# Kernel optimization log

Measured on AMD Instinct MI355X. Metric: run time of the kernel, lower is better.

## Reference

```python
import jax, jax.numpy as jnp
import numpy as np

N = 100000
E = 1600000
F_DIM = 128
H_DIM = 64
K_CLUSTERS = 16
NEG_SLOPE = 0.2


def setup_inputs() -> dict:
    key = jax.random.key(0)
    ks = jax.random.split(key, 10)
    X = jax.random.normal(ks[0], (N, F_DIM), dtype=jnp.float32)
    ei_feat = jax.random.randint(ks[1], (2, E), 0, N, dtype=jnp.int64)
    batch = jnp.zeros((N,), dtype=jnp.int64)
    # GATv2Conv layer 1 params (heads=1): lin_l, lin_r [F,H], att [H], bias [H]
    s1 = 1.0 / np.sqrt(F_DIM)
    W1l = jax.random.uniform(ks[2], (F_DIM, H_DIM), jnp.float32, -s1, s1)
    W1r = jax.random.uniform(ks[3], (F_DIM, H_DIM), jnp.float32, -s1, s1)
    a1 = jax.random.uniform(ks[4], (H_DIM,), jnp.float32, -1/np.sqrt(H_DIM), 1/np.sqrt(H_DIM))
    b1 = jnp.zeros((H_DIM,), jnp.float32)
    # layer 2: [H,K]
    s2 = 1.0 / np.sqrt(H_DIM)
    W2l = jax.random.uniform(ks[5], (H_DIM, K_CLUSTERS), jnp.float32, -s2, s2)
    W2r = jax.random.uniform(ks[6], (H_DIM, K_CLUSTERS), jnp.float32, -s2, s2)
    a2 = jax.random.uniform(ks[7], (K_CLUSTERS,), jnp.float32, -1/np.sqrt(K_CLUSTERS), 1/np.sqrt(K_CLUSTERS))
    b2 = jnp.zeros((K_CLUSTERS,), jnp.float32)
    return {"X": X, "ei_feat": ei_feat, "batch": batch,
            "W1l": W1l, "W1r": W1r, "a1": a1, "b1": b1,
            "W2l": W2l, "W2r": W2r, "a2": a2, "b2": b2}


def gatv2_conv(x, src, dst, Wl, Wr, a, b, n_nodes):
    # GATv2 (heads=1): e_ij = a^T LeakyReLU(Wl x_j + Wr x_i); softmax over j->i; out_i = sum alpha * Wl x_j
    xl = x @ Wl            # [N,H] source transform
    xr = x @ Wr            # [N,H] target transform
    e = jax.nn.leaky_relu(xl[src] + xr[dst], NEG_SLOPE) @ a   # [E']
    m = jax.ops.segment_max(e, dst, num_segments=n_nodes)      # stable softmax per target
    w = jnp.exp(e - m[dst])
    denom = jax.ops.segment_sum(w, dst, num_segments=n_nodes)
    alpha = w / denom[dst]  # every node has a self-loop, so denom > 0
    out = jax.ops.segment_sum(alpha[:, None] * xl[src], dst, num_segments=n_nodes)
    return out + b


def reference(X, ei_feat, batch, W1l, W1r, a1, b1, W2l, W2r, a2, b2):
    loop = jnp.arange(N, dtype=ei_feat.dtype)
    src = jnp.concatenate([ei_feat[0], loop])  # add_self_loops=True (PyG default)
    dst = jnp.concatenate([ei_feat[1], loop])
    h = jax.nn.elu(gatv2_conv(X, src, dst, W1l, W1r, a1, b1, N))
    z = gatv2_conv(h, src, dst, W2l, W2r, a2, b2, N)
    return jax.nn.softmax(z, axis=1)
```

## Files before the change

### kernel.cpp

```cpp
#include <hip/hip_runtime.h>
#include <stdint.h>

#define F_DIM 128
#define H_DIM 64
#define K_DIM 16
#define BUK_SH 8
#define NCH 256

typedef _Float16 half2v __attribute__((ext_vector_type(2)));
typedef _Float16 half4 __attribute__((ext_vector_type(4)));
typedef _Float16 f16x8 __attribute__((ext_vector_type(8)));
typedef float f32x4 __attribute__((ext_vector_type(4)));

__global__ __launch_bounds__(256) void k_hist(const int* __restrict__ dst,
                                              int* __restrict__ hist,
                                              int E, int CH, int NBUK) {
    __shared__ int h[512];
    int t = threadIdx.x, c = blockIdx.x;
    for (int i = t; i < NBUK; i += 256) h[i] = 0;
    __syncthreads();
    int s = c * CH, e = min(s + CH, E);
    for (int i = s + t; i < e; i += 256) atomicAdd(&h[dst[i] >> BUK_SH], 1);
    __syncthreads();
    for (int i = t; i < NBUK; i += 256) hist[i * NCH + c] = h[i];
}

__global__ __launch_bounds__(256) void k_scanBkt(int* __restrict__ hist,
                                                 int* __restrict__ bktTot) {
    __shared__ int sh[256];
    int b = blockIdx.x, t = threadIdx.x;
    int v = hist[b * NCH + t];
    sh[t] = v;
    __syncthreads();
    for (int off = 1; off < 256; off <<= 1) {
        int x = (t >= off) ? sh[t - off] : 0;
        __syncthreads();
        sh[t] += x;
        __syncthreads();
    }
    hist[b * NCH + t] = sh[t] - v;
    if (t == 255) bktTot[b] = sh[255];
}

__global__ __launch_bounds__(256) void k_scanTot(const int* __restrict__ bktTot,
                                                 int* __restrict__ bktBase, int NBUK) {
    __shared__ int sh[256];
    int t = threadIdx.x;
    int i0 = 2 * t, i1 = 2 * t + 1;
    int v0 = (i0 < NBUK) ? bktTot[i0] : 0;
    int v1 = (i1 < NBUK) ? bktTot[i1] : 0;
    int s = v0 + v1;
    sh[t] = s;
    __syncthreads();
    for (int off = 1; off < 256; off <<= 1) {
        int x = (t >= off) ? sh[t - off] : 0;
        __syncthreads();
        sh[t] += x;
        __syncthreads();
    }
    int excl = sh[t] - s;
    if (i0 < NBUK) bktBase[i0] = excl;
    if (i1 < NBUK) bktBase[i1] = excl + v0;
    if (t == 255) bktBase[NBUK] = sh[255];
}

__global__ __launch_bounds__(256) void k_scatter(const int* __restrict__ src,
                                                 const int* __restrict__ dst,
                                                 const int* __restrict__ hist,
                                                 const int* __restrict__ bktBase,
                                                 uint32_t* __restrict__ binned,
                                                 int E, int CH, int NBUK) {
    __shared__ int ctr[512];
    int t = threadIdx.x, c = blockIdx.x;
    for (int i = t; i < NBUK; i += 256) ctr[i] = bktBase[i] + hist[i * NCH + c];
    __syncthreads();
    int s = c * CH, e = min(s + CH, E);
    for (int i = s + t; i < e; i += 256) {
        int d = dst[i];
        int pos = atomicAdd(&ctr[d >> BUK_SH], 1);
        binned[pos] = (uint32_t)src[i] | ((uint32_t)(d & 255) << 20);
    }
}

__global__ __launch_bounds__(256) void k_fine2(const uint32_t* __restrict__ binned,
                                               const int* __restrict__ bktBase,
                                               int* __restrict__ rowptr,
                                               int* __restrict__ col, int N) {
    __shared__ int h[256], sc[256], slotL[256];
    int b = blockIdx.x, t = threadIdx.x;
    int n0 = b << BUK_SH;
    int s = bktBase[b], e = bktBase[b + 1];
    h[t] = 0;
    __syncthreads();
    for (int i = s + t; i < e; i += 256) atomicAdd(&h[binned[i] >> 20], 1);
    __syncthreads();
    int v = h[t];
    sc[t] = v;
    __syncthreads();
    for (int off = 1; off < 256; off <<= 1) {
        int x = (t >= off) ? sc[t - off] : 0;
        __syncthreads();
        sc[t] += x;
        __syncthreads();
    }
    int excl = sc[t] - v;
    int n = n0 + t;
    int rowbase = s + n0;
    if (n < N) {
        int rp = rowbase + excl + t;
        rowptr[n] = rp;
        col[rp] = n;
        slotL[t] = rp + 1;
        if (n == N - 1) rowptr[N] = rp + v + 1;
    }
    __syncthreads();
    for (int i = s + t; i < e; i += 256) {
        uint32_t p = binned[i];
        int pos = atomicAdd(&slotL[p >> 20], 1);
        col[pos] = (int)(p & 0xFFFFFu);
    }
}

__global__ __launch_bounds__(256) void k_gemm1m(
        const float* __restrict__ X,
        const float* __restrict__ W1l, const float* __restrict__ W1r,
        _Float16* __restrict__ xlh, _Float16* __restrict__ xrh, int N) {
    __shared__ _Float16 Ws[16384];
    __shared__ _Float16 Xs[128 * 136];
    int t = threadIdx.x;
    int n0 = blockIdx.x * 128;
    int validRows = N - n0; if (validRows > 128) validRows = 128;
    for (int i = t; i < 4096; i += 256) {
        int k = i >> 5, c4 = (i & 31) << 2;
        float4 v = (c4 < 64) ? *(const float4*)&W1l[k * 64 + c4]
                             : *(const float4*)&W1r[k * 64 + (c4 - 64)];
        int s = k >> 5, q = (k >> 3) & 3, j = k & 7;
        float vv[4] = {v.x, v.y, v.z, v.w};
#pragma unroll
        for (int u = 0; u < 4; ++u) {
            int C = c4 + u, c = C >> 4, n = C & 15;
            Ws[(((c * 4 + s) * 4 + q) * 16 + n) * 8 + j] = (_Float16)vv[u];
        }
    }
    for (int i = t; i < 4096; i += 256) {
        int r = i >> 5, c4 = (i & 31) << 2;
        float4 v = {0.f, 0.f, 0.f, 0.f};
        if (r < validRows) v = *(const float4*)&X[(long)(n0 + r) * 128 + c4];
        half4 hv;
        hv.x = (_Float16)v.x; hv.y = (_Float16)v.y;
        hv.z = (_Float16)v.z; hv.w = (_Float16)v.w;
        *(half4*)&Xs[r * 136 + c4] = hv;
    }
    __syncthreads();
    int w = t >> 6, lane = t & 63;
    int m = lane & 15, q = lane >> 4;
    f32x4 acc[2][8];
#pragma unroll
    for (int a = 0; a < 2; ++a)
#pragma unroll
        for (int c = 0; c < 8; ++c) acc[a][c] = (f32x4){0.f, 0.f, 0.f, 0.f};
#pragma unroll
    for (int s = 0; s < 4; ++s) {
        f16x8 a0 = *(const f16x8*)&Xs[(w * 32 + m) * 136 + s * 32 + q * 8];
        f16x8 a1 = *(const f16x8*)&Xs[(w * 32 + 16 + m) * 136 + s * 32 + q * 8];
#pragma unroll
        for (int c = 0; c < 8; ++c) {
            f16x8 b = *(const f16x8*)&Ws[(((c * 4 + s) * 4 + q) * 16 + m) * 8];
            acc[0][c] = __builtin_amdgcn_mfma_f32_16x16x32_f16(a0, b, acc[0][c], 0, 0, 0);
            acc[1][c] = __builtin_amdgcn_mfma_f32_16x16x32_f16(a1, b, acc[1][c], 0, 0, 0);
        }
    }
#pragma unroll
    for (int sub = 0; sub < 2; ++sub)
#pragma unroll
    for (int c = 0; c < 8; ++c)
#pragma unroll
    for (int r = 0; r < 4; ++r) {
        int gn = n0 + w * 32 + sub * 16 + q * 4 + r;
        if (gn < N) {
            int C = c * 16 + m;
            _Float16 v = (_Float16)acc[sub][c][r];
            if (C < 64) xlh[(long)gn * 64 + C] = v;
            else        xrh[(long)gn * 64 + (C - 64)] = v;
        }
    }
}

__global__ __launch_bounds__(256) void k_gemm2m(
        const _Float16* __restrict__ Hm,
        const float* __restrict__ W2l, const float* __restrict__ W2r,
        _Float16* __restrict__ xlh, _Float16* __restrict__ xrh, int N) {
    __shared__ _Float16 Ws2[2048];
    __shared__ _Float16 Hs[256 * 72];
    int t = threadIdx.x;
    int n0 = blockIdx.x * 256;
    int validRows = N - n0; if (validRows > 256) validRows = 256;
    for (int i = t; i < 512; i += 256) {
        int k = i >> 3, c4 = (i & 7) << 2;
        float4 v = (c4 < 16) ? *(const float4*)&W2l[k * 16 + c4]
                             : *(const float4*)&W2r[k * 16 + (c4 - 16)];
        int s = k >> 5, q = (k >> 3) & 3, j = k & 7;
        float vv[4] = {v.x, v.y, v.z, v.w};
#pragma unroll
        for (int u = 0; u < 4; ++u) {
            int C = c4 + u, c = C >> 4, n = C & 15;
            Ws2[(((c * 2 + s) * 4 + q) * 16 + n) * 8 + j] = (_Float16)vv[u];
        }
    }
    for (int i = t; i < 2048; i += 256) {
        int r = i >> 3, c8 = (i & 7) << 3;
        f16x8 v = {0, 0, 0, 0, 0, 0, 0, 0};
        if (r < validRows) v = *(const f16x8*)&Hm[(long)(n0 + r) * 64 + c8];
        *(f16x8*)&Hs[r * 72 + c8] = v;
    }
    __syncthreads();
    int w = t >> 6, lane = t & 63;
    int m = lane & 15, q = lane >> 4;
    f32x4 acc[4][2];
#pragma unroll
    for (int a = 0; a < 4; ++a)
#pragma unroll
        for (int c = 0; c < 2; ++c) acc[a][c] = (f32x4){0.f, 0.f, 0.f, 0.f};
#pragma unroll
    for (int s = 0; s < 2; ++s) {
        f16x8 a[4];
#pragma unroll
        for (int sub = 0; sub < 4; ++sub)
            a[sub] = *(const f16x8*)&Hs[(w * 64 + sub * 16 + m) * 72 + s * 32 + q * 8];
#pragma unroll
        for (int c = 0; c < 2; ++c) {
            f16x8 b = *(const f16x8*)&Ws2[(((c * 2 + s) * 4 + q) * 16 + m) * 8];
#pragma unroll
            for (int sub = 0; sub < 4; ++sub)
                acc[sub][c] = __builtin_amdgcn_mfma_f32_16x16x32_f16(a[sub], b, acc[sub][c], 0, 0, 0);
        }
    }
#pragma unroll
    for (int sub = 0; sub < 4; ++sub)
#pragma unroll
    for (int c = 0; c < 2; ++c)
#pragma unroll
    for (int r = 0; r < 4; ++r) {
        int gn = n0 + w * 64 + sub * 16 + q * 4 + r;
        if (gn < N) {
            int C = c * 16 + m;
            _Float16 v = (_Float16)acc[sub][c][r];
            if (C < 16) xlh[(long)gn * 16 + C] = v;
            else        xrh[(long)gn * 16 + (C - 16)] = v;
        }
    }
}

__global__ void k_att1(const f16x8* __restrict__ xlh, const f16x8* __restrict__ xrh,
                       const float* __restrict__ a1, const float* __restrict__ b1,
                       const int* __restrict__ rowptr, const int* __restrict__ col,
                       f16x8* __restrict__ hout, int N) {
    int n = (int)((blockIdx.x * (unsigned)blockDim.x + threadIdx.x) >> 6);
    int lane = threadIdx.x & 63;
    if (n >= N) return;
    int q = lane & 7;
    int g = lane >> 3;
    float4 af0 = ((const float4*)a1)[q * 2 + 0];
    float4 af1 = ((const float4*)a1)[q * 2 + 1];
    half2v a01 = {(_Float16)af0.x, (_Float16)af0.y};
    half2v a23 = {(_Float16)af0.z, (_Float16)af0.w};
    half2v a45 = {(_Float16)af1.x, (_Float16)af1.y};
    half2v a67 = {(_Float16)af1.z, (_Float16)af1.w};
    f16x8 xrv = xrh[(long)n * 8 + q];
    int jb = rowptr[n], je = rowptr[n + 1];
    float l = 0.f;
    float o[8] = {0.f, 0.f, 0.f, 0.f, 0.f, 0.f, 0.f, 0.f};
    int j = jb + g;
    for (; j + 8 < je; j += 16) {
        int s0 = col[j], s1 = col[j + 8];
        f16x8 xh0 = xlh[(long)s0 * 8 + q];
        f16x8 xh1 = xlh[(long)s1 * 8 + q];
        f16x8 t0 = xh0 + xrv, t1 = xh1 + xrv;
        f16x8 u0 = __builtin_elementwise_max(t0, t0 * (_Float16)0.2f);
        f16x8 u1 = __builtin_elementwise_max(t1, t1 * (_Float16)0.2f);
        half2v u0a = {u0[0], u0[1]}, u0b = {u0[2], u0[3]}, u0c = {u0[4], u0[5]}, u0d = {u0[6], u0[7]};
        half2v u1a = {u1[0], u1[1]}, u1b = {u1[2], u1[3]}, u1c = {u1[4], u1[5]}, u1d = {u1[6], u1[7]};
        float e0 = __builtin_amdgcn_fdot2(u0a, a01,
                    __builtin_amdgcn_fdot2(u0b, a23,
                     __builtin_amdgcn_fdot2(u0c, a45,
                      __builtin_amdgcn_fdot2(u0d, a67, 0.f, false), false), false), false);
        float e1 = __builtin_amdgcn_fdot2(u1a, a01,
                    __builtin_amdgcn_fdot2(u1b, a23,
                     __builtin_amdgcn_fdot2(u1c, a45,
                      __builtin_amdgcn_fdot2(u1d, a67, 0.f, false), false), false), false);
#pragma unroll
        for (int off = 1; off < 8; off <<= 1) {
            e0 += __shfl_xor(e0, off, 8);
            e1 += __shfl_xor(e1, off, 8);
        }
        float c0 = __expf(e0), c1 = __expf(e1);
        l += c0 + c1;
#pragma unroll
        for (int i = 0; i < 8; ++i)
            o[i] = fmaf(c0, (float)xh0[i], fmaf(c1, (float)xh1[i], o[i]));
    }
    for (; j < je; j += 8) {
        int s = col[j];
        f16x8 xh = xlh[(long)s * 8 + q];
        f16x8 t = xh + xrv;
        f16x8 u = __builtin_elementwise_max(t, t * (_Float16)0.2f);
        half2v ua = {u[0], u[1]}, ub = {u[2], u[3]}, uc = {u[4], u[5]}, ud = {u[6], u[7]};
        float e = __builtin_amdgcn_fdot2(ua, a01,
                   __builtin_amdgcn_fdot2(ub, a23,
                    __builtin_amdgcn_fdot2(uc, a45,
                     __builtin_amdgcn_fdot2(ud, a67, 0.f, false), false), false), false);
#pragma unroll
        for (int off = 1; off < 8; off <<= 1) e += __shfl_xor(e, off, 8);
        float c = __expf(e);
        l += c;
#pragma unroll
        for (int i = 0; i < 8; ++i) o[i] = fmaf(c, (float)xh[i], o[i]);
    }
#pragma unroll
    for (int off = 8; off <= 32; off <<= 1) {
        l += __shfl_xor(l, off);
#pragma unroll
        for (int i = 0; i < 8; ++i) o[i] += __shfl_xor(o[i], off);
    }
    if (g == 0) {
        float4 bv0 = ((const float4*)b1)[q * 2 + 0];
        float4 bv1 = ((const float4*)b1)[q * 2 + 1];
        float bb[8] = {bv0.x, bv0.y, bv0.z, bv0.w, bv1.x, bv1.y, bv1.z, bv1.w};
        float rl = 1.f / l;
        f16x8 hv;
#pragma unroll
        for (int i = 0; i < 8; ++i) {
            float h = o[i] * rl + bb[i];
            h = (h > 0.f) ? h : (__expf(h) - 1.f);
            hv[i] = (_Float16)h;
        }
        hout[(long)n * 8 + q] = hv;
    }
}

__global__ void k_att2(const half4* __restrict__ xlh, const half4* __restrict__ xrh,
                       const float* __restrict__ a2, const float* __restrict__ b2v,
                       const int* __restrict__ rowptr, const int* __restrict__ col,
                       float* __restrict__ out, int N) {
    int n = (int)((blockIdx.x * (unsigned)blockDim.x + threadIdx.x) >> 6);
    int lane = threadIdx.x & 63;
    if (n >= N) return;
    int q = lane & 3;
    int g = lane >> 2;
    float4 af = ((const float4*)a2)[q];
    half2v alo = {(_Float16)af.x, (_Float16)af.y};
    half2v ahi = {(_Float16)af.z, (_Float16)af.w};
    half4 xrv = xrh[(long)n * 4 + q];
    int jb = rowptr[n], je = rowptr[n + 1];
    float l = 0.f;
    float4 o = {0.f, 0.f, 0.f, 0.f};
    for (int j = jb + g; j < je; j += 16) {
        int s = col[j];
        half4 xh = xlh[(long)s * 4 + q];
        half4 t = xh + xrv;
        half4 u = __builtin_elementwise_max(t, t * (_Float16)0.2f);
        half2v ulo = {u.x, u.y}, uhi = {u.z, u.w};
        float e = __builtin_amdgcn_fdot2(ulo, alo,
                   __builtin_amdgcn_fdot2(uhi, ahi, 0.f, false), false);
        e += __shfl_xor(e, 1, 4);
        e += __shfl_xor(e, 2, 4);
        float c = __expf(e);
        l += c;
        o.x = fmaf(c, (float)xh.x, o.x);
        o.y = fmaf(c, (float)xh.y, o.y);
        o.z = fmaf(c, (float)xh.z, o.z);
        o.w = fmaf(c, (float)xh.w, o.w);
    }
#pragma unroll
    for (int off = 4; off <= 32; off <<= 1) {
        l   += __shfl_xor(l, off);
        o.x += __shfl_xor(o.x, off);
        o.y += __shfl_xor(o.y, off);
        o.z += __shfl_xor(o.z, off);
        o.w += __shfl_xor(o.w, off);
    }
    if (g == 0) {
        float4 bv = ((const float4*)b2v)[q];
        float rl = 1.f / l;
        float4 z;
        z.x = o.x * rl + bv.x;
        z.y = o.y * rl + bv.y;
        z.z = o.z * rl + bv.z;
        z.w = o.w * rl + bv.w;
        float mx = fmaxf(fmaxf(z.x, z.y), fmaxf(z.z, z.w));
        mx = fmaxf(mx, __shfl_xor(mx, 1, 4));
        mx = fmaxf(mx, __shfl_xor(mx, 2, 4));
        float4 ez;
        ez.x = __expf(z.x - mx); ez.y = __expf(z.y - mx);
        ez.z = __expf(z.z - mx); ez.w = __expf(z.w - mx);
        float ss = ez.x + ez.y + ez.z + ez.w;
        ss += __shfl_xor(ss, 1, 4);
        ss += __shfl_xor(ss, 2, 4);
        float rs = 1.f / ss;
        ez.x *= rs; ez.y *= rs; ez.z *= rs; ez.w *= rs;
        ((float4*)out)[(long)n * 4 + q] = ez;
    }
}

extern "C" void kernel_launch(void* const* d_in, const int* in_sizes, int n_in,
                              void* d_out, int out_size, void* d_ws, size_t ws_size,
                              hipStream_t stream) {
    const float* X   = (const float*)d_in[0];
    const int*   ei  = (const int*)d_in[1];
    const float* W1l = (const float*)d_in[3];
    const float* W1r = (const float*)d_in[4];
    const float* a1  = (const float*)d_in[5];
    const float* b1  = (const float*)d_in[6];
    const float* W2l = (const float*)d_in[7];
    const float* W2r = (const float*)d_in[8];
    const float* a2  = (const float*)d_in[9];
    const float* b2  = (const float*)d_in[10];

    int N = in_sizes[0] / F_DIM;
    int E = in_sizes[1] / 2;
    int M = E + N;
    int NBUK = (N + 255) >> BUK_SH;
    int NH = NBUK * NCH;
    int CH = (E + NCH - 1) / NCH;
    const int* srcv = ei;
    const int* dstv = ei + E;

    char* w = (char*)d_ws;
    size_t off = 0;
    auto alloc = [&](size_t bytes) -> char* {
        char* p = w + off;
        off = (off + bytes + 255) & ~(size_t)255;
        return p;
    };
    int* rowptr  = (int*)alloc((size_t)(N + 1) * sizeof(int));
    int* hist    = (int*)alloc((size_t)NH * sizeof(int));
    int* bktTot  = (int*)alloc((size_t)NBUK * sizeof(int));
    int* bktBase = (int*)alloc((size_t)(NBUK + 1) * sizeof(int));
    int* col     = (int*)alloc((size_t)M * sizeof(int));
    uint32_t* binned = (uint32_t*)alloc((size_t)E * sizeof(uint32_t));
    _Float16* xl1h = (_Float16*)alloc((size_t)N * H_DIM * 2);
    _Float16* xr1h = (_Float16*)alloc((size_t)N * H_DIM * 2);
    _Float16* h1h  = (_Float16*)alloc((size_t)N * H_DIM * 2);
    _Float16* xl2h = (_Float16*)alloc((size_t)N * K_DIM * 2);
    _Float16* xr2h = (_Float16*)alloc((size_t)N * K_DIM * 2);

    k_hist<<<NCH, 256, 0, stream>>>(dstv, hist, E, CH, NBUK);
    k_scanBkt<<<NBUK, 256, 0, stream>>>(hist, bktTot);
    k_scanTot<<<1, 256, 0, stream>>>(bktTot, bktBase, NBUK);
    k_scatter<<<NCH, 256, 0, stream>>>(srcv, dstv, hist, bktBase, binned, E, CH, NBUK);
    k_fine2<<<NBUK, 256, 0, stream>>>(binned, bktBase, rowptr, col, N);

    int g1Blocks = (N + 127) / 128;
    k_gemm1m<<<g1Blocks, 256, 0, stream>>>(X, W1l, W1r, xl1h, xr1h, N);
    int nodeBlocks = (N + 3) / 4;
    k_att1<<<nodeBlocks, 256, 0, stream>>>((const f16x8*)xl1h, (const f16x8*)xr1h,
                                           a1, b1, rowptr, col, (f16x8*)h1h, N);
    int g2Blocks = (N + 255) / 256;
    k_gemm2m<<<g2Blocks, 256, 0, stream>>>(h1h, W2l, W2r, xl2h, xr2h, N);
    k_att2<<<nodeBlocks, 256, 0, stream>>>((const half4*)xl2h, (const half4*)xr2h,
                                           a2, b2, rowptr, col, (float*)d_out, N);
}
```

Measured before the change: 292.2 us.

## Map each node to 16 lanes instead of a full wavefront in attention kernels

Both GATv2 attention kernels now give each destination node 16 lanes instead of 64, so one wavefront processes four nodes. In layer 1 that is 2 edge groups of 8 lanes; in layer 2 it is 4 groups of 4 lanes, and the layer-2 loop is also unrolled 2-way. Average degree is about 17, so the old 64-lane mapping left most edge groups idle and spent many shuffle steps on the cross-group reduction. The new mapping cuts idle lanes and reduction work, but each lane group now walks a longer serial edge loop and load balance across nodes is coarser.

Measured after the change: 247.1 us. 1.18x faster.

```diff
diff --git a/kernel.cpp b/kernel.cpp
--- a/kernel.cpp
+++ b/kernel.cpp
@@ -255,11 +255,11 @@
                        const float* __restrict__ a1, const float* __restrict__ b1,
                        const int* __restrict__ rowptr, const int* __restrict__ col,
                        f16x8* __restrict__ hout, int N) {
-    int n = (int)((blockIdx.x * (unsigned)blockDim.x + threadIdx.x) >> 6);
+    int n = (int)((blockIdx.x * (unsigned)blockDim.x + threadIdx.x) >> 4);
     int lane = threadIdx.x & 63;
     if (n >= N) return;
     int q = lane & 7;
-    int g = lane >> 3;
+    int g = (lane >> 3) & 1;
     float4 af0 = ((const float4*)a1)[q * 2 + 0];
     float4 af1 = ((const float4*)a1)[q * 2 + 1];
     half2v a01 = {(_Float16)af0.x, (_Float16)af0.y};
@@ -271,8 +271,8 @@
     float l = 0.f;
     float o[8] = {0.f, 0.f, 0.f, 0.f, 0.f, 0.f, 0.f, 0.f};
     int j = jb + g;
-    for (; j + 8 < je; j += 16) {
-        int s0 = col[j], s1 = col[j + 8];
+    for (; j + 2 < je; j += 4) {
+        int s0 = col[j], s1 = col[j + 2];
         f16x8 xh0 = xlh[(long)s0 * 8 + q];
         f16x8 xh1 = xlh[(long)s1 * 8 + q];
         f16x8 t0 = xh0 + xrv, t1 = xh1 + xrv;
@@ -299,7 +299,7 @@
         for (int i = 0; i < 8; ++i)
             o[i] = fmaf(c0, (float)xh0[i], fmaf(c1, (float)xh1[i], o[i]));
     }
-    for (; j < je; j += 8) {
+    for (; j < je; j += 2) {
         int s = col[j];
         f16x8 xh = xlh[(long)s * 8 + q];
         f16x8 t = xh + xrv;
@@ -316,12 +316,9 @@
 #pragma unroll
         for (int i = 0; i < 8; ++i) o[i] = fmaf(c, (float)xh[i], o[i]);
     }
-#pragma unroll
-    for (int off = 8; off <= 32; off <<= 1) {
-        l += __shfl_xor(l, off);
-#pragma unroll
-        for (int i = 0; i < 8; ++i) o[i] += __shfl_xor(o[i], off);
-    }
+    l += __shfl_xor(l, 8);
+#pragma unroll
+    for (int i = 0; i < 8; ++i) o[i] += __shfl_xor(o[i], 8);
     if (g == 0) {
         float4 bv0 = ((const float4*)b1)[q * 2 + 0];
         float4 bv1 = ((const float4*)b1)[q * 2 + 1];
@@ -342,11 +339,11 @@
                        const float* __restrict__ a2, const float* __restrict__ b2v,
                        const int* __restrict__ rowptr, const int* __restrict__ col,
                        float* __restrict__ out, int N) {
-    int n = (int)((blockIdx.x * (unsigned)blockDim.x + threadIdx.x) >> 6);
+    int n = (int)((blockIdx.x * (unsigned)blockDim.x + threadIdx.x) >> 4);
     int lane = threadIdx.x & 63;
     if (n >= N) return;
     int q = lane & 3;
-    int g = lane >> 2;
+    int g = (lane >> 2) & 3;
     float4 af = ((const float4*)a2)[q];
     half2v alo = {(_Float16)af.x, (_Float16)af.y};
     half2v ahi = {(_Float16)af.z, (_Float16)af.w};
@@ -354,7 +351,30 @@
     int jb = rowptr[n], je = rowptr[n + 1];
     float l = 0.f;
     float4 o = {0.f, 0.f, 0.f, 0.f};
-    for (int j = jb + g; j < je; j += 16) {
+    int j = jb + g;
+    for (; j + 4 < je; j += 8) {
+        int s0 = col[j], s1 = col[j + 4];
+        half4 xh0 = xlh[(long)s0 * 4 + q];
+        half4 xh1 = xlh[(long)s1 * 4 + q];
+        half4 t0 = xh0 + xrv, t1 = xh1 + xrv;
+        half4 u0 = __builtin_elementwise_max(t0, t0 * (_Float16)0.2f);
+        half4 u1 = __builtin_elementwise_max(t1, t1 * (_Float16)0.2f);
+        half2v u0lo = {u0.x, u0.y}, u0hi = {u0.z, u0.w};
+        half2v u1lo = {u1.x, u1.y}, u1hi = {u1.z, u1.w};
+        float e0 = __builtin_amdgcn_fdot2(u0lo, alo,
+                    __builtin_amdgcn_fdot2(u0hi, ahi, 0.f, false), false);
+        float e1 = __builtin_amdgcn_fdot2(u1lo, alo,
+                    __builtin_amdgcn_fdot2(u1hi, ahi, 0.f, false), false);
+        e0 += __shfl_xor(e0, 1, 4); e0 += __shfl_xor(e0, 2, 4);
+        e1 += __shfl_xor(e1, 1, 4); e1 += __shfl_xor(e1, 2, 4);
+        float c0 = __expf(e0), c1 = __expf(e1);
+        l += c0 + c1;
+        o.x = fmaf(c0, (float)xh0.x, fmaf(c1, (float)xh1.x, o.x));
+        o.y = fmaf(c0, (float)xh0.y, fmaf(c1, (float)xh1.y, o.y));
+        o.z = fmaf(c0, (float)xh0.z, fmaf(c1, (float)xh1.z, o.z));
+        o.w = fmaf(c0, (float)xh0.w, fmaf(c1, (float)xh1.w, o.w));
+    }
+    for (; j < je; j += 4) {
         int s = col[j];
         half4 xh = xlh[(long)s * 4 + q];
         half4 t = xh + xrv;
@@ -372,7 +392,7 @@
         o.w = fmaf(c, (float)xh.w, o.w);
     }
 #pragma unroll
-    for (int off = 4; off <= 32; off <<= 1) {
+    for (int off = 4; off <= 8; off <<= 1) {
         l   += __shfl_xor(l, off);
         o.x += __shfl_xor(o.x, off);
         o.y += __shfl_xor(o.y, off);
@@ -452,11 +472,11 @@
 
     int g1Blocks = (N + 127) / 128;
     k_gemm1m<<<g1Blocks, 256, 0, stream>>>(X, W1l, W1r, xl1h, xr1h, N);
-    int nodeBlocks = (N + 3) / 4;
-    k_att1<<<nodeBlocks, 256, 0, stream>>>((const f16x8*)xl1h, (const f16x8*)xr1h,
-                                           a1, b1, rowptr, col, (f16x8*)h1h, N);
+    int nodeBlocks16 = (N + 15) / 16;
+    k_att1<<<nodeBlocks16, 256, 0, stream>>>((const f16x8*)xl1h, (const f16x8*)xr1h,
+                                             a1, b1, rowptr, col, (f16x8*)h1h, N);
     int g2Blocks = (N + 255) / 256;
     k_gemm2m<<<g2Blocks, 256, 0, stream>>>(h1h, W2l, W2r, xl2h, xr2h, N);
-    k_att2<<<nodeBlocks, 256, 0, stream>>>((const half4*)xl2h, (const half4*)xr2h,
-                                           a2, b2, rowptr, col, (float*)d_out, N);
-}
+    k_att2<<<nodeBlocks16, 256, 0, stream>>>((const half4*)xl2h, (const half4*)xr2h,
+                                             a2, b2, rowptr, col, (float*)d_out, N);
+}
```
